# Performance work log

Hardware: AMD Instinct MI355X
Metric: run time of the kernel (lower is better)

## Reference

```python
import jax, jax.numpy as jnp
import numpy as np

B, N, D = 16, 8192, 64
M, S = 256, 32          # npoints, nsample
OUT = 128
RADIUS = 0.4
WC = 64                 # WeightNet output channels
BN_EPS = 1e-5
_BN_SCALE = 1.0 / np.sqrt(1.0 + BN_EPS)  # eval-mode BN, running mean 0 / var 1


def _bn(x, gamma, beta):
    shp = [1] * x.ndim
    shp[1] = -1
    return gamma.reshape(shp) * (x * _BN_SCALE) + beta.reshape(shp)


def _pdist2(a, b):
    # a (B,P,3), b (B,Q,3) -> (B,P,Q) squared distances
    return (jnp.sum(a * a, -1)[:, :, None] + jnp.sum(b * b, -1)[:, None, :]
            - 2.0 * jnp.einsum('bpd,bqd->bpq', a, b))


def _fps(xyz, npoints):
    # furthest point sampling, pointnet2 semantics (start at index 0)
    Bq, Nq, _ = xyz.shape
    first = jnp.zeros((Bq,), jnp.int32)

    def step(carry, _):
        dist, last = carry
        pt = xyz[jnp.arange(Bq), last]                   # (B,3)
        d = jnp.sum((xyz - pt[:, None, :]) ** 2, -1)
        dist = jnp.minimum(dist, d)
        nxt = jnp.argmax(dist, -1).astype(jnp.int32)
        return (dist, nxt), nxt

    init = (jnp.full((Bq, Nq), 1e10, xyz.dtype), first)
    _, rest = jax.lax.scan(step, init, None, length=npoints - 1)
    return jnp.concatenate([first[None], rest], 0).T     # (B, npoints)


def _ball_query(xyz, new_xyz, radius, nsample):
    # first `nsample` indices within radius, pad by repeating first valid index
    d2 = _pdist2(new_xyz, xyz)                           # (B,M,N)
    n = xyz.shape[1]
    key = jnp.where(d2 <= radius * radius, n - jnp.arange(n, dtype=jnp.int32), 0)
    vals, idx = jax.lax.top_k(key, nsample)              # lowest in-radius indices first
    return jnp.where(vals > 0, idx, idx[:, :, :1])


def _group(x_ch, idx):
    # x_ch (B,C,N), idx (B,M,S) -> (B,C,M,S)
    return jax.vmap(lambda f, i: f[:, i])(x_ch, idx)


def setup_inputs():
    key = jax.random.key(0)
    ks = jax.random.split(key, 8)
    f = jnp.float32

    def w(k, o, i):
        return (jax.random.normal(k, (o, i), f) / np.sqrt(i)).astype(f)

    return {
        'xyz': jax.random.uniform(ks[0], (B, N, 3), f),
        'feature': jax.random.normal(ks[1], (B, D, N), f),
        'w0': w(ks[2], WC, 3), 'b0': jnp.zeros((WC,), f), 'gamma0': jnp.ones((WC,), f), 'beta0': jnp.zeros((WC,), f),
        'w1': w(ks[3], WC, WC), 'b1': jnp.zeros((WC,), f), 'gamma1': jnp.ones((WC,), f), 'beta1': jnp.zeros((WC,), f),
        'w2': w(ks[4], WC, WC), 'b2': jnp.zeros((WC,), f),
        'wl': w(ks[5], OUT, D * WC), 'bl': jnp.zeros((OUT,), f), 'gammal': jnp.ones((OUT,), f), 'betal': jnp.zeros((OUT,), f),
        'wf': w(ks[6], OUT, D + OUT), 'bf': jnp.zeros((OUT,), f), 'gammaf': jnp.ones((OUT,), f), 'betaf': jnp.zeros((OUT,), f),
    }


def reference(xyz, feature, w0, b0, gamma0, beta0, w1, b1, gamma1, beta1, w2, b2,
              wl, bl, gammal, betal, wf, bf, gammaf, betaf):
    relu = jax.nn.relu
    # ---- furthest point sampling ----
    fidx = _fps(xyz, M)                                  # (B,M)
    new_xyz = xyz[jnp.arange(B)[:, None], fidx]          # (B,M,3)
    # ---- ball query + grouping ----
    gidx = _ball_query(xyz, new_xyz, RADIUS, S)          # (B,M,S)
    xyz_ch = jnp.transpose(xyz, (0, 2, 1))               # (B,3,N)
    grouped_xyz = _group(xyz_ch, gidx) - jnp.transpose(new_xyz, (0, 2, 1))[:, :, :, None]  # (B,3,M,S) centered
    grouped_feat = _group(feature, gidx)                 # (B,D,M,S)
    # ---- WeightNet (1x1 convs on offsets) ----
    h = relu(_bn(jnp.einsum('oc,bcms->boms', w0, grouped_xyz) + b0[None, :, None, None], gamma0, beta0))
    h = relu(_bn(jnp.einsum('oc,bcms->boms', w1, h) + b1[None, :, None, None], gamma1, beta1))
    weights = jnp.einsum('oc,bcms->boms', w2, h) + b2[None, :, None, None]  # (B,WC,M,S)
    # ---- weighted aggregation: (B,M,D,S) @ (B,M,S,WC) -> (B,M,D*WC) ----
    agg = jnp.einsum('bdms,bwms->bmdw', grouped_feat, weights).reshape(B, M, D * WC)
    new_feature = relu(_bn(jnp.einsum('od,bmd->bom', wl, agg) + bl[None, :, None], gammal, betal))  # (B,OUT,M)
    # ---- three-NN interpolation back to N points ----
    d2 = _pdist2(xyz, new_xyz)                           # (B,N,M)
    negd, nidx = jax.lax.top_k(-d2, 3)                   # 3 nearest sampled centers
    rd = 1.0 / (-negd + 1e-8)                            # reverse density on squared distance
    wts = rd / jnp.sum(rd, -1, keepdims=True)            # (B,N,3)
    gathered = jax.vmap(lambda f2, i: f2[:, i])(new_feature, nidx)  # (B,OUT,N,3)
    interp = jnp.einsum('bcnk,bnk->bcn', gathered, wts)  # (B,OUT,N)
    # ---- concat skip + final 1x1 conv ----
    cat = jnp.concatenate([interp, feature], 1)          # (B,OUT+D,N)
    return relu(_bn(jnp.einsum('oc,bcn->bon', wf, cat) + bf[None, :, None], gammaf, betaf))
```

## Files before the change

kernel.cpp:

```cpp
#include <hip/hip_runtime.h>
#include <cstdint>
#include <cstddef>

#define BB   16
#define NN   8192
#define DD   64
#define MM   256
#define SS   32
#define OUTC 128
#define WCC  64

__device__ __forceinline__ float bnf(float x, float g, float be){
    const float BNS = 0.99999500003749969f;
    return g * (x * BNS) + be;
}

__global__ __launch_bounds__(256) void k_tf(const float* __restrict__ f, float* __restrict__ fT){
  const int blk = blockIdx.x;
  const int b  = blk >> 7;
  const int n0 = (blk & 127) << 6;
  __shared__ float tile[64][65];
  const int t = threadIdx.x;
  {
    const int d = t >> 2, j0 = (t & 3) << 4;
    const float* src = f + ((size_t)b*DD + d)*NN + n0 + j0;
#pragma unroll
    for (int i=0;i<16;i+=4){
      float4 v = *(const float4*)(src + i);
      tile[d][j0+i+0]=v.x; tile[d][j0+i+1]=v.y; tile[d][j0+i+2]=v.z; tile[d][j0+i+3]=v.w;
    }
  }
  __syncthreads();
  {
    const int j = t >> 2, d0 = (t & 3) << 4;
    float* dst = fT + ((size_t)b*NN + n0 + j)*DD + d0;
#pragma unroll
    for (int i=0;i<16;i+=4){
      float4 v = make_float4(tile[d0+i][j], tile[d0+i+1][j], tile[d0+i+2][j], tile[d0+i+3][j]);
      *(float4*)(dst + i) = v;
    }
  }
}

__global__ __launch_bounds__(256) void k_twl(const float* __restrict__ wl, float* __restrict__ wlT){
  int idx = blockIdx.x*256 + threadIdx.x;
  if (idx < 4096*OUTC){
    int k = idx >> 7, o = idx & 127;
    wlT[idx] = wl[(size_t)o*4096 + k];
  }
}
__global__ __launch_bounds__(256) void k_twf(const float* __restrict__ wf, float* __restrict__ wfT){
  int idx = blockIdx.x*256 + threadIdx.x;
  if (idx < 192*OUTC){
    int k = idx >> 7, o = idx & 127;
    wfT[idx] = wf[o*192 + k];
  }
}

__global__ __launch_bounds__(256) void k_fps(const float* __restrict__ xyz,
                                             float* __restrict__ nxyz){
  const int b = blockIdx.x;
  const int t = threadIdx.x;
  const float* xb = xyz + (size_t)b*NN*3;
  __shared__ float sxyz[NN*3];
  __shared__ float snew[MM*3];
  __shared__ unsigned long long skey[2][4];
  for (int i = t; i < NN*3; i += 256) sxyz[i] = xb[i];
  float px[32], py[32], pz[32], dist[32];
#pragma unroll
  for (int i=0;i<32;i++){
    int id = i*256 + t;
    px[i] = xb[id*3+0]; py[i] = xb[id*3+1]; pz[i] = xb[id*3+2];
    dist[i] = 1e10f;
  }
  __syncthreads();
  float lx = sxyz[0], ly = sxyz[1], lz = sxyz[2];
  if (t==0){ snew[0]=lx; snew[1]=ly; snew[2]=lz; }
  for (int step=1; step<MM; ++step){
    float bv = 0.0f; int bi = NN-1;
#pragma unroll
    for (int i=0;i<32;i++){
      float dx=px[i]-lx, dy=py[i]-ly, dz=pz[i]-lz;
      float d = dx*dx + dy*dy + dz*dz;
      float nd = fminf(dist[i], d);
      dist[i] = nd;
      bool gt = nd > bv;
      bv = gt ? nd : bv;
      bi = gt ? (i*256 + t) : bi;
    }
    unsigned long long key = ((unsigned long long)__float_as_uint(bv) << 32) | (unsigned)(NN-1 - bi);
#pragma unroll
    for (int off=1; off<64; off<<=1){
      unsigned long long ok = __shfl_xor(key, off, 64);
      if (ok > key) key = ok;
    }
    const int p = step & 1;
    if ((t & 63) == 0) skey[p][t>>6] = key;
    __syncthreads();
    unsigned long long k0=skey[p][0], k1=skey[p][1], k2=skey[p][2], k3=skey[p][3];
    unsigned long long ka = k0>k1?k0:k1, kb = k2>k3?k2:k3;
    unsigned long long kw = ka>kb?ka:kb;
    const int bid = (NN-1) - (int)(unsigned)(kw & 0xFFFFFFFFull);
    lx = sxyz[bid*3+0]; ly = sxyz[bid*3+1]; lz = sxyz[bid*3+2];
    if (t==0){ snew[step*3+0]=lx; snew[step*3+1]=ly; snew[step*3+2]=lz; }
  }
  __syncthreads();
  for (int i = t; i < MM*3; i += 256) nxyz[(size_t)b*MM*3 + i] = snew[i];
}

__global__ __launch_bounds__(64) void k_bq_mlp(const float* __restrict__ xyz,
    const float* __restrict__ nxyz,
    const float* __restrict__ w0, const float* __restrict__ b0,
    const float* __restrict__ g0, const float* __restrict__ be0,
    const float* __restrict__ w1, const float* __restrict__ b1,
    const float* __restrict__ g1, const float* __restrict__ be1,
    const float* __restrict__ w2, const float* __restrict__ b2,
    int* __restrict__ gidx, float* __restrict__ wbuf){
  const int bm = blockIdx.x;
  const int b  = bm >> 8;
  const int c  = threadIdx.x;
  __shared__ int   sidx[SS];
  __shared__ float sgx[3][SS];
  __shared__ float sh0[SS][WCC];
  __shared__ float sh1[SS][WCC];

  const float w0r0 = w0[c*3+0], w0r1 = w0[c*3+1], w0r2 = w0[c*3+2];
  const float b0c=b0[c], g0c=g0[c], be0c=be0[c];
  const float b1c=b1[c], g1c=g1[c], be1c=be1[c], b2c=b2[c];
  float w1r[64], w2r[64];
#pragma unroll
  for (int i=0;i<16;i++){
    float4 v = *(const float4*)(w1 + c*64 + i*4);
    w1r[i*4+0]=v.x; w1r[i*4+1]=v.y; w1r[i*4+2]=v.z; w1r[i*4+3]=v.w;
    float4 u = *(const float4*)(w2 + c*64 + i*4);
    w2r[i*4+0]=u.x; w2r[i*4+1]=u.y; w2r[i*4+2]=u.z; w2r[i*4+3]=u.w;
  }
  const float cx = nxyz[bm*3+0], cy = nxyz[bm*3+1], cz = nxyz[bm*3+2];
  const float* xb = xyz + (size_t)b*NN*3;
  const float R2 = (float)(0.4*0.4);
  int cnt = 0;
  for (int n0=0; n0<NN && cnt<SS; n0+=64){
    int n = n0 + c;
    float dx = xb[n*3+0]-cx, dy = xb[n*3+1]-cy, dz = xb[n*3+2]-cz;
    float d2 = dx*dx+dy*dy+dz*dz;
    bool in = (d2 <= R2);
    unsigned long long mk = __ballot(in);
    int rank = cnt + (int)__popcll(mk & ((1ull<<c)-1ull));
    if (in && rank < SS) sidx[rank] = n;
    cnt += (int)__popcll(mk);
  }
  int total = min(cnt, SS);
  __syncthreads();
  int i0 = sidx[0];
  if (c >= total && c < SS) sidx[c] = i0;
  __syncthreads();
  if (c < SS){
    int p = sidx[c];
    gidx[bm*SS + c] = p;
    sgx[0][c] = xb[p*3+0]-cx;
    sgx[1][c] = xb[p*3+1]-cy;
    sgx[2][c] = xb[p*3+2]-cz;
  }
  __syncthreads();
  for (int s=0;s<SS;s++){
    float pre = w0r0*sgx[0][s] + w0r1*sgx[1][s] + w0r2*sgx[2][s] + b0c;
    sh0[s][c] = fmaxf(bnf(pre, g0c, be0c), 0.f);
  }
  __syncthreads();
  for (int s=0;s<SS;s++){
    float a = b1c;
#pragma unroll
    for (int k=0;k<64;k+=4){
      float4 h = *(const float4*)(&sh0[s][k]);
      a += w1r[k]*h.x + w1r[k+1]*h.y + w1r[k+2]*h.z + w1r[k+3]*h.w;
    }
    sh1[s][c] = fmaxf(bnf(a, g1c, be1c), 0.f);
  }
  __syncthreads();
  float* wb = wbuf + (size_t)bm*SS*WCC;
  for (int s=0;s<SS;s++){
    float a = b2c;
#pragma unroll
    for (int k=0;k<64;k+=4){
      float4 h = *(const float4*)(&sh1[s][k]);
      a += w2r[k]*h.x + w2r[k+1]*h.y + w2r[k+2]*h.z + w2r[k+3]*h.w;
    }
    wb[s*WCC + c] = a;
  }
}

__global__ __launch_bounds__(256) void k_agg(const float* __restrict__ featT,
                                             const float* __restrict__ wbuf,
                                             const int* __restrict__ gidx,
                                             float* __restrict__ agg){
  const int bm = blockIdx.x;
  const int b  = bm >> 8;
  __shared__ float wt[SS][WCC];
  __shared__ int   sidx[SS];
  const int t = threadIdx.x;
  const float* wsrc = wbuf + (size_t)bm*SS*WCC;
#pragma unroll
  for (int i=0;i<8;i++){
    int li = t + i*256;
    ((float*)wt)[li] = wsrc[li];
  }
  if (t < SS) sidx[t] = gidx[bm*SS + t];
  __syncthreads();
  const int d  = t & 63;
  const int wg = t >> 6;
  float acc[16];
#pragma unroll
  for (int j=0;j<16;j++) acc[j]=0.f;
  const float* fb = featT + (size_t)b*NN*DD;
  for (int s=0;s<SS;s++){
    float fv = fb[(size_t)sidx[s]*DD + d];
#pragma unroll
    for (int j=0;j<16;j++) acc[j] += fv * wt[s][wg*16+j];
  }
  float* ab = agg + (size_t)bm*4096 + d*64 + wg*16;
#pragma unroll
  for (int j=0;j<16;j+=4){
    *(float4*)(ab+j) = make_float4(acc[j],acc[j+1],acc[j+2],acc[j+3]);
  }
}

__global__ __launch_bounds__(256) void k_nf_part(const float* __restrict__ agg, const float* __restrict__ wlT,
    float* __restrict__ part){
  const int blk = blockIdx.x;
  const int rb  = blk >> 2;
  const int ks  = blk & 3;
  const int row0 = rb * 64;
  const int kbase = ks * 1024;
  __shared__ float As[64][65];
  __shared__ float Bs[64][128];
  const int t = threadIdx.x;
  float acc[4][8];
#pragma unroll
  for (int i=0;i<4;i++)
#pragma unroll
    for (int j=0;j<8;j++) acc[i][j]=0.f;
  const int mg = t >> 4, og = t & 15;
  for (int k0=kbase; k0<kbase+1024; k0+=64){
    {
      const int r = t >> 2, c0 = (t & 3) << 4;
      const float* src = agg + (size_t)(row0 + r)*4096 + k0 + c0;
#pragma unroll
      for (int i=0;i<16;i+=4){
        float4 v = *(const float4*)(src+i);
        As[r][c0+i+0]=v.x; As[r][c0+i+1]=v.y; As[r][c0+i+2]=v.z; As[r][c0+i+3]=v.w;
      }
    }
#pragma unroll
    for (int ch=0; ch<8; ch++){
      int li = ch*1024 + t*4;
      int kk = li >> 7, o = li & 127;
      float4 v = *(const float4*)(wlT + (size_t)(k0+kk)*128 + o);
      *(float4*)(&Bs[kk][o]) = v;
    }
    __syncthreads();
#pragma unroll 8
    for (int kk=0; kk<64; kk++){
      float a0 = As[mg*4+0][kk], a1 = As[mg*4+1][kk], a2 = As[mg*4+2][kk], a3 = As[mg*4+3][kk];
      float4 bA = *(float4*)(&Bs[kk][og*8]);
      float4 bB = *(float4*)(&Bs[kk][og*8+4]);
      float bb[8] = {bA.x,bA.y,bA.z,bA.w,bB.x,bB.y,bB.z,bB.w};
#pragma unroll
      for (int j=0;j<8;j++){
        acc[0][j] += a0*bb[j];
        acc[1][j] += a1*bb[j];
        acc[2][j] += a2*bb[j];
        acc[3][j] += a3*bb[j];
      }
    }
    __syncthreads();
  }
  float* pb = part + ((size_t)ks << 19);
#pragma unroll
  for (int i=0;i<4;i++){
    const int row = row0 + mg*4 + i;
    float* dst = pb + (size_t)row*128 + og*8;
    *(float4*)(dst)   = make_float4(acc[i][0],acc[i][1],acc[i][2],acc[i][3]);
    *(float4*)(dst+4) = make_float4(acc[i][4],acc[i][5],acc[i][6],acc[i][7]);
  }
}

__global__ __launch_bounds__(256) void k_nf_ep(const float* __restrict__ part,
    const float* __restrict__ bl, const float* __restrict__ gl, const float* __restrict__ bel,
    float* __restrict__ nfT){
  const int gid = blockIdx.x*256 + threadIdx.x;
  const int base = gid*4;
  const int o0 = base & 127;
  float4 s0 = *(const float4*)(part + base);
  float4 s1 = *(const float4*)(part + (1<<19) + base);
  float4 s2 = *(const float4*)(part + (2<<19) + base);
  float4 s3 = *(const float4*)(part + (3<<19) + base);
  float sum[4] = {s0.x+s1.x+s2.x+s3.x, s0.y+s1.y+s2.y+s3.y,
                  s0.z+s1.z+s2.z+s3.z, s0.w+s1.w+s2.w+s3.w};
  float ov[4];
#pragma unroll
  for (int j=0;j<4;j++){
    const int o = o0 + j;
    ov[j] = fmaxf(bnf(sum[j] + bl[o], gl[o], bel[o]), 0.f);
  }
  *(float4*)(nfT + base) = make_float4(ov[0],ov[1],ov[2],ov[3]);
}

__global__ __launch_bounds__(256) void k_3nn(const float* __restrict__ xyz, const float* __restrict__ nxyz,
    const float* __restrict__ nfT, float* __restrict__ interpT){
  const int blk = blockIdx.x;
  const int b  = blk >> 5;
  const int n0 = (blk & 31) << 8;
  __shared__ float snew[MM][3];
  __shared__ float sw[256][3];
  __shared__ int   si[256][3];
  const int t = threadIdx.x;
  if (t < 192){
    float4 v = *(const float4*)(nxyz + (size_t)b*MM*3 + t*4);
    ((float*)snew)[t*4+0]=v.x; ((float*)snew)[t*4+1]=v.y; ((float*)snew)[t*4+2]=v.z; ((float*)snew)[t*4+3]=v.w;
  }
  __syncthreads();
  {
    const int n = n0 + t;
    const float x = xyz[((size_t)b*NN+n)*3+0];
    const float y = xyz[((size_t)b*NN+n)*3+1];
    const float z = xyz[((size_t)b*NN+n)*3+2];
    float d1=1e30f, d2=1e30f, d3=1e30f; int i1=0,i2=0,i3=0;
    for (int m=0;m<MM;m++){
      float dx=x-snew[m][0], dy=y-snew[m][1], dz=z-snew[m][2];
      float d = dx*dx+dy*dy+dz*dz;
      if (d < d3){
        if (d < d1){ d3=d2;i3=i2; d2=d1;i2=i1; d1=d;i1=m; }
        else if (d < d2){ d3=d2;i3=i2; d2=d;i2=m; }
        else { d3=d;i3=m; }
      }
    }
    float r1=1.f/(d1+1e-8f), r2=1.f/(d2+1e-8f), r3=1.f/(d3+1e-8f);
    float rs = 1.f/(r1+r2+r3);
    sw[t][0]=r1*rs; sw[t][1]=r2*rs; sw[t][2]=r3*rs;
    si[t][0]=i1; si[t][1]=i2; si[t][2]=i3;
  }
  __syncthreads();
  const int c = t & 127, half = t >> 7;
  for (int r=0;r<128;r++){
    const int nn = r*2 + half;
    const float w0v=sw[nn][0], w1v=sw[nn][1], w2v=sw[nn][2];
    const float* p0 = nfT + ((size_t)b*MM + si[nn][0])*128;
    const float* p1 = nfT + ((size_t)b*MM + si[nn][1])*128;
    const float* p2 = nfT + ((size_t)b*MM + si[nn][2])*128;
    interpT[((size_t)b*NN + n0 + nn)*128 + c] = w0v*p0[c] + w1v*p1[c] + w2v*p2[c];
  }
}

__global__ __launch_bounds__(256) void k_final(const float* __restrict__ interpT, const float* __restrict__ feature,
    const float* __restrict__ wfT,
    const float* __restrict__ bf, const float* __restrict__ gf, const float* __restrict__ bef,
    float* __restrict__ out){
  const int blk = blockIdx.x;
  const int b  = blk >> 6;
  const int n0 = (blk & 63) << 7;
  __shared__ float Wsh[32][128];
  __shared__ float Csh[32][132];
  const int t = threadIdx.x;
  float acc[8][8];
#pragma unroll
  for (int i=0;i<8;i++)
#pragma unroll
    for (int j=0;j<8;j++) acc[i][j]=0.f;
  const int og = t >> 4, ng = t & 15;
  for (int k0=0; k0<192; k0+=32){
    {
      const int kk = t >> 3, o0 = (t & 7) << 4;
#pragma unroll
      for (int i=0;i<16;i+=4)
        *(float4*)(&Wsh[kk][o0+i]) = *(const float4*)(wfT + (size_t)(k0+kk)*128 + o0 + i);
    }
    if (k0 < 128){
      const int nn = t >> 1, kb = (t & 1) << 4;
      const float* src = interpT + ((size_t)b*NN + n0 + nn)*128 + k0 + kb;
#pragma unroll
      for (int i=0;i<16;i+=4){
        float4 v = *(const float4*)(src+i);
        Csh[kb+i+0][nn]=v.x; Csh[kb+i+1][nn]=v.y; Csh[kb+i+2][nn]=v.z; Csh[kb+i+3][nn]=v.w;
      }
    } else {
      const int kk = t >> 3, nb = (t & 7) << 4;
      const float* src = feature + ((size_t)b*DD + (k0-128) + kk)*NN + n0 + nb;
#pragma unroll
      for (int i=0;i<16;i+=4){
        float4 v = *(const float4*)(src+i);
        *(float4*)(&Csh[kk][nb+i]) = v;
      }
    }
    __syncthreads();
#pragma unroll 8
    for (int kk=0;kk<32;kk++){
      float4 a0 = *(float4*)(&Wsh[kk][og*8]);
      float4 a1 = *(float4*)(&Wsh[kk][og*8+4]);
      float av[8] = {a0.x,a0.y,a0.z,a0.w,a1.x,a1.y,a1.z,a1.w};
      float4 c0 = *(float4*)(&Csh[kk][ng*8]);
      float4 c1 = *(float4*)(&Csh[kk][ng*8+4]);
      float cv[8] = {c0.x,c0.y,c0.z,c0.w,c1.x,c1.y,c1.z,c1.w};
#pragma unroll
      for (int i=0;i<8;i++)
#pragma unroll
        for (int j=0;j<8;j++)
          acc[i][j] += av[i]*cv[j];
    }
    __syncthreads();
  }
#pragma unroll
  for (int i=0;i<8;i++){
    const int o = og*8 + i;
    const float bfo = bf[o], gfo = gf[o], befo = bef[o];
    float ov[8];
#pragma unroll
    for (int j=0;j<8;j++) ov[j] = fmaxf(bnf(acc[i][j] + bfo, gfo, befo), 0.f);
    float* dst = out + ((size_t)b*OUTC + o)*NN + n0 + ng*8;
    *(float4*)(dst)   = make_float4(ov[0],ov[1],ov[2],ov[3]);
    *(float4*)(dst+4) = make_float4(ov[4],ov[5],ov[6],ov[7]);
  }
}

extern "C" void kernel_launch(void* const* d_in, const int* in_sizes, int n_in,
                              void* d_out, int out_size, void* d_ws, size_t ws_size,
                              hipStream_t stream){
  const float* xyz     = (const float*)d_in[0];
  const float* feature = (const float*)d_in[1];
  const float* w0  = (const float*)d_in[2];
  const float* b0  = (const float*)d_in[3];
  const float* g0  = (const float*)d_in[4];
  const float* be0 = (const float*)d_in[5];
  const float* w1  = (const float*)d_in[6];
  const float* b1  = (const float*)d_in[7];
  const float* g1  = (const float*)d_in[8];
  const float* be1 = (const float*)d_in[9];
  const float* w2  = (const float*)d_in[10];
  const float* b2  = (const float*)d_in[11];
  const float* wl  = (const float*)d_in[12];
  const float* bl  = (const float*)d_in[13];
  const float* gl  = (const float*)d_in[14];
  const float* bel = (const float*)d_in[15];
  const float* wf  = (const float*)d_in[16];
  const float* bf  = (const float*)d_in[17];
  const float* gf  = (const float*)d_in[18];
  const float* bef = (const float*)d_in[19];
  float* out = (float*)d_out;

  char* ws = (char*)d_ws;
  float* featT = (float*)(ws + 0);
  float* wbuf  = (float*)(ws + 33554432);
  float* part  = (float*)(ws + 33554432);
  float* agg   = (float*)(ws + 67108864);
  float* wlT   = (float*)(ws + 134217728);
  float* wfT   = (float*)(ws + 136314880);
  float* nxyz  = (float*)(ws + 136429568);
  int*   gidx  = (int*)  (ws + 136478720);
  float* nfT   = (float*)(ws + 137003008);
  float* interpT = (float*)(ws + 0);

  k_tf     <<<2048, 256, 0, stream>>>(feature, featT);
  k_twl    <<<2048, 256, 0, stream>>>(wl, wlT);
  k_twf    <<<96,   256, 0, stream>>>(wf, wfT);
  k_fps    <<<BB,   256, 0, stream>>>(xyz, nxyz);
  k_bq_mlp <<<BB*MM, 64, 0, stream>>>(xyz, nxyz, w0,b0,g0,be0, w1,b1,g1,be1, w2,b2, gidx, wbuf);
  k_agg    <<<BB*MM, 256, 0, stream>>>(featT, wbuf, gidx, agg);
  k_nf_part<<<256,  256, 0, stream>>>(agg, wlT, part);
  k_nf_ep  <<<512,  256, 0, stream>>>(part, bl, gl, bel, nfT);
  k_3nn    <<<BB*(NN/256), 256, 0, stream>>>(xyz, nxyz, nfT, interpT);
  k_final  <<<BB*(NN/128), 256, 0, stream>>>(interpT, feature, wfT, bf, gf, bef, out);
}
```

Before: 642.1 us.

## Use bf16 MFMA for linear layer, fuse 3-NN into final conv, widen FPS

The big 4096-wide linear layer now uses bf16 inputs and 16x16x32 bf16 MFMA instructions instead of an fp32 shared-memory FMA GEMM. The aggregation kernel writes bf16 output, and the weight conversion kernel turns wl into bf16 without transposing it. The 3-NN interpolation is fused into the final 1x1 conv, which removes the interpT round trip and one launch. FPS now runs with 512 threads per block to shorten each thread's serial loop. bf16 lowers precision on a 4096-long reduction, which may push results out of tolerance.

```diff
diff --git a/kernel.cpp b/kernel.cpp
--- a/kernel.cpp
+++ b/kernel.cpp
@@ -1,4 +1,5 @@
 #include <hip/hip_runtime.h>
+#include <hip/hip_bf16.h>
 #include <cstdint>
 #include <cstddef>
 
@@ -10,9 +11,16 @@
 #define OUTC 128
 #define WCC  64
 
+using short8 = __attribute__((ext_vector_type(8))) short;
+using f32x4  = __attribute__((ext_vector_type(4))) float;
+
 __device__ __forceinline__ float bnf(float x, float g, float be){
     const float BNS = 0.99999500003749969f;
     return g * (x * BNS) + be;
+}
+__device__ __forceinline__ unsigned short f2bf(float f){
+    __hip_bfloat16 h = __float2bfloat16(f);
+    return *reinterpret_cast<unsigned short*>(&h);
 }
 
 __global__ __launch_bounds__(256) void k_tf(const float* __restrict__ f, float* __restrict__ fT){
@@ -42,12 +50,11 @@
   }
 }
 
-__global__ __launch_bounds__(256) void k_twl(const float* __restrict__ wl, float* __restrict__ wlT){
-  int idx = blockIdx.x*256 + threadIdx.x;
-  if (idx < 4096*OUTC){
-    int k = idx >> 7, o = idx & 127;
-    wlT[idx] = wl[(size_t)o*4096 + k];
-  }
+__global__ __launch_bounds__(256) void k_twl(const float* __restrict__ wl, unsigned short* __restrict__ wlB){
+  int idx = (blockIdx.x*256 + threadIdx.x)*4;
+  float4 v = *(const float4*)(wl + idx);
+  ushort4 h = make_ushort4(f2bf(v.x), f2bf(v.y), f2bf(v.z), f2bf(v.w));
+  *(ushort4*)(wlB + idx) = h;
 }
 __global__ __launch_bounds__(256) void k_twf(const float* __restrict__ wf, float* __restrict__ wfT){
   int idx = blockIdx.x*256 + threadIdx.x;
@@ -57,19 +64,19 @@
   }
 }
 
-__global__ __launch_bounds__(256) void k_fps(const float* __restrict__ xyz,
+__global__ __launch_bounds__(512) void k_fps(const float* __restrict__ xyz,
                                              float* __restrict__ nxyz){
   const int b = blockIdx.x;
   const int t = threadIdx.x;
   const float* xb = xyz + (size_t)b*NN*3;
   __shared__ float sxyz[NN*3];
   __shared__ float snew[MM*3];
-  __shared__ unsigned long long skey[2][4];
-  for (int i = t; i < NN*3; i += 256) sxyz[i] = xb[i];
-  float px[32], py[32], pz[32], dist[32];
-#pragma unroll
-  for (int i=0;i<32;i++){
-    int id = i*256 + t;
+  __shared__ unsigned long long skey[2][8];
+  for (int i = t; i < NN*3; i += 512) sxyz[i] = xb[i];
+  float px[16], py[16], pz[16], dist[16];
+#pragma unroll
+  for (int i=0;i<16;i++){
+    int id = i*512 + t;
     px[i] = xb[id*3+0]; py[i] = xb[id*3+1]; pz[i] = xb[id*3+2];
     dist[i] = 1e10f;
   }
@@ -79,14 +86,14 @@
   for (int step=1; step<MM; ++step){
     float bv = 0.0f; int bi = NN-1;
 #pragma unroll
-    for (int i=0;i<32;i++){
+    for (int i=0;i<16;i++){
       float dx=px[i]-lx, dy=py[i]-ly, dz=pz[i]-lz;
       float d = dx*dx + dy*dy + dz*dz;
       float nd = fminf(dist[i], d);
       dist[i] = nd;
       bool gt = nd > bv;
       bv = gt ? nd : bv;
-      bi = gt ? (i*256 + t) : bi;
+      bi = gt ? (i*512 + t) : bi;
     }
     unsigned long long key = ((unsigned long long)__float_as_uint(bv) << 32) | (unsigned)(NN-1 - bi);
 #pragma unroll
@@ -98,14 +105,17 @@
     if ((t & 63) == 0) skey[p][t>>6] = key;
     __syncthreads();
     unsigned long long k0=skey[p][0], k1=skey[p][1], k2=skey[p][2], k3=skey[p][3];
-    unsigned long long ka = k0>k1?k0:k1, kb = k2>k3?k2:k3;
-    unsigned long long kw = ka>kb?ka:kb;
+    unsigned long long k4=skey[p][4], k5=skey[p][5], k6=skey[p][6], k7=skey[p][7];
+    unsigned long long ka = k0>k1?k0:k1, kb2 = k2>k3?k2:k3;
+    unsigned long long kc = k4>k5?k4:k5, kd = k6>k7?k6:k7;
+    unsigned long long ke = ka>kb2?ka:kb2, kf = kc>kd?kc:kd;
+    unsigned long long kw = ke>kf?ke:kf;
     const int bid = (NN-1) - (int)(unsigned)(kw & 0xFFFFFFFFull);
     lx = sxyz[bid*3+0]; ly = sxyz[bid*3+1]; lz = sxyz[bid*3+2];
     if (t==0){ snew[step*3+0]=lx; snew[step*3+1]=ly; snew[step*3+2]=lz; }
   }
   __syncthreads();
-  for (int i = t; i < MM*3; i += 256) nxyz[(size_t)b*MM*3 + i] = snew[i];
+  for (int i = t; i < MM*3; i += 512) nxyz[(size_t)b*MM*3 + i] = snew[i];
 }
 
 __global__ __launch_bounds__(64) void k_bq_mlp(const float* __restrict__ xyz,
@@ -192,7 +202,7 @@
 __global__ __launch_bounds__(256) void k_agg(const float* __restrict__ featT,
                                              const float* __restrict__ wbuf,
                                              const int* __restrict__ gidx,
-                                             float* __restrict__ agg){
+                                             unsigned short* __restrict__ aggB){
   const int bm = blockIdx.x;
   const int b  = bm >> 8;
   __shared__ float wt[SS][WCC];
@@ -217,70 +227,45 @@
 #pragma unroll
     for (int j=0;j<16;j++) acc[j] += fv * wt[s][wg*16+j];
   }
-  float* ab = agg + (size_t)bm*4096 + d*64 + wg*16;
-#pragma unroll
-  for (int j=0;j<16;j+=4){
-    *(float4*)(ab+j) = make_float4(acc[j],acc[j+1],acc[j+2],acc[j+3]);
-  }
-}
-
-__global__ __launch_bounds__(256) void k_nf_part(const float* __restrict__ agg, const float* __restrict__ wlT,
-    float* __restrict__ part){
+  unsigned short h[16];
+#pragma unroll
+  for (int j=0;j<16;j++) h[j] = f2bf(acc[j]);
+  unsigned short* ab = aggB + (size_t)bm*4096 + d*64 + wg*16;
+  *(uint4*)(ab)     = *(uint4*)(&h[0]);
+  *(uint4*)(ab + 8) = *(uint4*)(&h[8]);
+}
+
+__global__ __launch_bounds__(256) void k_nf_part(const unsigned short* __restrict__ aggB,
+                                                 const unsigned short* __restrict__ wlB,
+                                                 float* __restrict__ part){
   const int blk = blockIdx.x;
   const int rb  = blk >> 2;
   const int ks  = blk & 3;
-  const int row0 = rb * 64;
-  const int kbase = ks * 1024;
-  __shared__ float As[64][65];
-  __shared__ float Bs[64][128];
-  const int t = threadIdx.x;
-  float acc[4][8];
-#pragma unroll
-  for (int i=0;i<4;i++)
-#pragma unroll
-    for (int j=0;j<8;j++) acc[i][j]=0.f;
-  const int mg = t >> 4, og = t & 15;
-  for (int k0=kbase; k0<kbase+1024; k0+=64){
-    {
-      const int r = t >> 2, c0 = (t & 3) << 4;
-      const float* src = agg + (size_t)(row0 + r)*4096 + k0 + c0;
-#pragma unroll
-      for (int i=0;i<16;i+=4){
-        float4 v = *(const float4*)(src+i);
-        As[r][c0+i+0]=v.x; As[r][c0+i+1]=v.y; As[r][c0+i+2]=v.z; As[r][c0+i+3]=v.w;
-      }
-    }
-#pragma unroll
-    for (int ch=0; ch<8; ch++){
-      int li = ch*1024 + t*4;
-      int kk = li >> 7, o = li & 127;
-      float4 v = *(const float4*)(wlT + (size_t)(k0+kk)*128 + o);
-      *(float4*)(&Bs[kk][o]) = v;
-    }
-    __syncthreads();
-#pragma unroll 8
-    for (int kk=0; kk<64; kk++){
-      float a0 = As[mg*4+0][kk], a1 = As[mg*4+1][kk], a2 = As[mg*4+2][kk], a3 = As[mg*4+3][kk];
-      float4 bA = *(float4*)(&Bs[kk][og*8]);
-      float4 bB = *(float4*)(&Bs[kk][og*8+4]);
-      float bb[8] = {bA.x,bA.y,bA.z,bA.w,bB.x,bB.y,bB.z,bB.w};
-#pragma unroll
-      for (int j=0;j<8;j++){
-        acc[0][j] += a0*bb[j];
-        acc[1][j] += a1*bb[j];
-        acc[2][j] += a2*bb[j];
-        acc[3][j] += a3*bb[j];
-      }
-    }
-    __syncthreads();
+  const int wid = threadIdx.x >> 6, lane = threadIdx.x & 63;
+  const int m0 = rb*64 + wid*16;
+  const int r  = lane & 15, kg = lane >> 4;
+  f32x4 acc[8];
+#pragma unroll
+  for (int i=0;i<8;i++) acc[i] = (f32x4){0.f,0.f,0.f,0.f};
+  const short* arow = (const short*)aggB + (size_t)(m0 + r)*4096 + ks*1024 + kg*8;
+  const short* brow = (const short*)wlB  + (size_t)r*4096        + ks*1024 + kg*8;
+#pragma unroll 4
+  for (int kc=0; kc<32; kc++){
+    short8 a = *(const short8*)(arow + kc*32);
+#pragma unroll
+    for (int ot=0; ot<8; ot++){
+      short8 bfr = *(const short8*)(brow + (size_t)ot*16*4096 + kc*32);
+      acc[ot] = __builtin_amdgcn_mfma_f32_16x16x32_bf16(a, bfr, acc[ot], 0, 0, 0);
+    }
   }
   float* pb = part + ((size_t)ks << 19);
 #pragma unroll
-  for (int i=0;i<4;i++){
-    const int row = row0 + mg*4 + i;
-    float* dst = pb + (size_t)row*128 + og*8;
-    *(float4*)(dst)   = make_float4(acc[i][0],acc[i][1],acc[i][2],acc[i][3]);
-    *(float4*)(dst+4) = make_float4(acc[i][4],acc[i][5],acc[i][6],acc[i][7]);
+  for (int ot=0; ot<8; ot++){
+#pragma unroll
+    for (int rr=0; rr<4; rr++){
+      int row = m0 + kg*4 + rr;
+      pb[(size_t)row*128 + ot*16 + r] = acc[ot][rr];
+    }
   }
 }
 
@@ -305,54 +290,9 @@
   *(float4*)(nfT + base) = make_float4(ov[0],ov[1],ov[2],ov[3]);
 }
 
-__global__ __launch_bounds__(256) void k_3nn(const float* __restrict__ xyz, const float* __restrict__ nxyz,
-    const float* __restrict__ nfT, float* __restrict__ interpT){
-  const int blk = blockIdx.x;
-  const int b  = blk >> 5;
-  const int n0 = (blk & 31) << 8;
-  __shared__ float snew[MM][3];
-  __shared__ float sw[256][3];
-  __shared__ int   si[256][3];
-  const int t = threadIdx.x;
-  if (t < 192){
-    float4 v = *(const float4*)(nxyz + (size_t)b*MM*3 + t*4);
-    ((float*)snew)[t*4+0]=v.x; ((float*)snew)[t*4+1]=v.y; ((float*)snew)[t*4+2]=v.z; ((float*)snew)[t*4+3]=v.w;
-  }
-  __syncthreads();
-  {
-    const int n = n0 + t;
-    const float x = xyz[((size_t)b*NN+n)*3+0];
-    const float y = xyz[((size_t)b*NN+n)*3+1];
-    const float z = xyz[((size_t)b*NN+n)*3+2];
-    float d1=1e30f, d2=1e30f, d3=1e30f; int i1=0,i2=0,i3=0;
-    for (int m=0;m<MM;m++){
-      float dx=x-snew[m][0], dy=y-snew[m][1], dz=z-snew[m][2];
-      float d = dx*dx+dy*dy+dz*dz;
-      if (d < d3){
-        if (d < d1){ d3=d2;i3=i2; d2=d1;i2=i1; d1=d;i1=m; }
-        else if (d < d2){ d3=d2;i3=i2; d2=d;i2=m; }
-        else { d3=d;i3=m; }
-      }
-    }
-    float r1=1.f/(d1+1e-8f), r2=1.f/(d2+1e-8f), r3=1.f/(d3+1e-8f);
-    float rs = 1.f/(r1+r2+r3);
-    sw[t][0]=r1*rs; sw[t][1]=r2*rs; sw[t][2]=r3*rs;
-    si[t][0]=i1; si[t][1]=i2; si[t][2]=i3;
-  }
-  __syncthreads();
-  const int c = t & 127, half = t >> 7;
-  for (int r=0;r<128;r++){
-    const int nn = r*2 + half;
-    const float w0v=sw[nn][0], w1v=sw[nn][1], w2v=sw[nn][2];
-    const float* p0 = nfT + ((size_t)b*MM + si[nn][0])*128;
-    const float* p1 = nfT + ((size_t)b*MM + si[nn][1])*128;
-    const float* p2 = nfT + ((size_t)b*MM + si[nn][2])*128;
-    interpT[((size_t)b*NN + n0 + nn)*128 + c] = w0v*p0[c] + w1v*p1[c] + w2v*p2[c];
-  }
-}
-
-__global__ __launch_bounds__(256) void k_final(const float* __restrict__ interpT, const float* __restrict__ feature,
-    const float* __restrict__ wfT,
+__global__ __launch_bounds__(256) void k_final(const float* __restrict__ xyz,
+    const float* __restrict__ nxyz, const float* __restrict__ nfT,
+    const float* __restrict__ feature, const float* __restrict__ wfT,
     const float* __restrict__ bf, const float* __restrict__ gf, const float* __restrict__ bef,
     float* __restrict__ out){
   const int blk = blockIdx.x;
@@ -360,13 +300,44 @@
   const int n0 = (blk & 63) << 7;
   __shared__ float Wsh[32][128];
   __shared__ float Csh[32][132];
+  __shared__ float snew[MM*3];
+  __shared__ float sw[128][3];
+  __shared__ int   si[128][3];
   const int t = threadIdx.x;
+  if (t < 192){
+    float4 v = *(const float4*)(nxyz + (size_t)b*MM*3 + t*4);
+    snew[t*4+0]=v.x; snew[t*4+1]=v.y; snew[t*4+2]=v.z; snew[t*4+3]=v.w;
+  }
+  __syncthreads();
+  if (t < 128){
+    const int n = n0 + t;
+    const float x = xyz[((size_t)b*NN+n)*3+0];
+    const float y = xyz[((size_t)b*NN+n)*3+1];
+    const float z = xyz[((size_t)b*NN+n)*3+2];
+    float d1=1e30f, d2=1e30f, d3=1e30f; int i1=0,i2=0,i3=0;
+    for (int m=0;m<MM;m++){
+      float dx=x-snew[m*3+0], dy=y-snew[m*3+1], dz=z-snew[m*3+2];
+      float d = dx*dx+dy*dy+dz*dz;
+      if (d < d3){
+        if (d < d1){ d3=d2;i3=i2; d2=d1;i2=i1; d1=d;i1=m; }
+        else if (d < d2){ d3=d2;i3=i2; d2=d;i2=m; }
+        else { d3=d;i3=m; }
+      }
+    }
+    float r1=1.f/(d1+1e-8f), r2=1.f/(d2+1e-8f), r3=1.f/(d3+1e-8f);
+    float rs = 1.f/(r1+r2+r3);
+    sw[t][0]=r1*rs; sw[t][1]=r2*rs; sw[t][2]=r3*rs;
+    si[t][0]=i1; si[t][1]=i2; si[t][2]=i3;
+  }
+  __syncthreads();
+
   float acc[8][8];
 #pragma unroll
   for (int i=0;i<8;i++)
 #pragma unroll
     for (int j=0;j<8;j++) acc[i][j]=0.f;
   const int og = t >> 4, ng = t & 15;
+  const float* nfb = nfT + (size_t)b*MM*128;
   for (int k0=0; k0<192; k0+=32){
     {
       const int kk = t >> 3, o0 = (t & 7) << 4;
@@ -375,12 +346,20 @@
         *(float4*)(&Wsh[kk][o0+i]) = *(const float4*)(wfT + (size_t)(k0+kk)*128 + o0 + i);
     }
     if (k0 < 128){
-      const int nn = t >> 1, kb = (t & 1) << 4;
-      const float* src = interpT + ((size_t)b*NN + n0 + nn)*128 + k0 + kb;
+      const int nn = t >> 1, kb0 = (t & 1) << 4;
+      const float w0v = sw[nn][0], w1v = sw[nn][1], w2v = sw[nn][2];
+      const float* p0 = nfb + (size_t)si[nn][0]*128 + k0 + kb0;
+      const float* p1 = nfb + (size_t)si[nn][1]*128 + k0 + kb0;
+      const float* p2 = nfb + (size_t)si[nn][2]*128 + k0 + kb0;
 #pragma unroll
       for (int i=0;i<16;i+=4){
-        float4 v = *(const float4*)(src+i);
-        Csh[kb+i+0][nn]=v.x; Csh[kb+i+1][nn]=v.y; Csh[kb+i+2][nn]=v.z; Csh[kb+i+3][nn]=v.w;
+        float4 a = *(const float4*)(p0+i);
+        float4 bq = *(const float4*)(p1+i);
+        float4 cq = *(const float4*)(p2+i);
+        Csh[kb0+i+0][nn] = w0v*a.x + w1v*bq.x + w2v*cq.x;
+        Csh[kb0+i+1][nn] = w0v*a.y + w1v*bq.y + w2v*cq.y;
+        Csh[kb0+i+2][nn] = w0v*a.z + w1v*bq.z + w2v*cq.z;
+        Csh[kb0+i+3][nn] = w0v*a.w + w1v*bq.w + w2v*cq.w;
       }
     } else {
       const int kk = t >> 3, nb = (t & 7) << 4;
@@ -447,25 +426,23 @@
   float* out = (float*)d_out;
 
   char* ws = (char*)d_ws;
-  float* featT = (float*)(ws + 0);
-  float* wbuf  = (float*)(ws + 33554432);
-  float* part  = (float*)(ws + 33554432);
-  float* agg   = (float*)(ws + 67108864);
-  float* wlT   = (float*)(ws + 134217728);
-  float* wfT   = (float*)(ws + 136314880);
-  float* nxyz  = (float*)(ws + 136429568);
-  int*   gidx  = (int*)  (ws + 136478720);
-  float* nfT   = (float*)(ws + 137003008);
-  float* interpT = (float*)(ws + 0);
+  float*          featT = (float*)(ws + 0);
+  float*          wbuf  = (float*)(ws + 33554432);
+  float*          part  = (float*)(ws + 33554432);
+  unsigned short* aggB  = (unsigned short*)(ws + 67108864);
+  unsigned short* wlB   = (unsigned short*)(ws + 134217728);
+  float*          wfT   = (float*)(ws + 136314880);
+  float*          nxyz  = (float*)(ws + 136429568);
+  int*            gidx  = (int*)  (ws + 136478720);
+  float*          nfT   = (float*)(ws + 137003008);
 
   k_tf     <<<2048, 256, 0, stream>>>(feature, featT);
-  k_twl    <<<2048, 256, 0, stream>>>(wl, wlT);
+  k_twl    <<<512,  256, 0, stream>>>(wl, wlB);
   k_twf    <<<96,   256, 0, stream>>>(wf, wfT);
-  k_fps    <<<BB,   256, 0, stream>>>(xyz, nxyz);
+  k_fps    <<<BB,   512, 0, stream>>>(xyz, nxyz);
   k_bq_mlp <<<BB*MM, 64, 0, stream>>>(xyz, nxyz, w0,b0,g0,be0, w1,b1,g1,be1, w2,b2, gidx, wbuf);
-  k_agg    <<<BB*MM, 256, 0, stream>>>(featT, wbuf, gidx, agg);
-  k_nf_part<<<256,  256, 0, stream>>>(agg, wlT, part);
+  k_agg    <<<BB*MM, 256, 0, stream>>>(featT, wbuf, gidx, aggB);
+  k_nf_part<<<256,  256, 0, stream>>>(aggB, wlB, part);
   k_nf_ep  <<<512,  256, 0, stream>>>(part, bl, gl, bel, nfT);
-  k_3nn    <<<BB*(NN/256), 256, 0, stream>>>(xyz, nxyz, nfT, interpT);
-  k_final  <<<BB*(NN/128), 256, 0, stream>>>(interpT, feature, wfT, bf, gf, bef, out);
-}
+  k_final  <<<BB*(NN/128), 256, 0, stream>>>(xyz, nxyz, nfT, feature, wfT, bf, gf, bef, out);
+}
```

Result: faster. 616.2 us (-4.0%).
